# Optimization experiments

Hardware: AMD Instinct MI355X
Metric: run time of the kernel (lower is better)

## Reference

```python
import jax, jax.numpy as jnp
import numpy as np
import math
from jax.ops import segment_sum

TOPK_RATIO = 0.1
CLUSTER_RATIO = 0.25
K_KNN = 10


def setup_inputs() -> dict:
    key = jax.random.key(0)
    ks = jax.random.split(key, 10)
    N, C, H, W = 8, 256, 100, 352
    sc = 0.02
    return {
        "spatial_features_2d": jax.random.normal(ks[0], (N, C, H, W), jnp.float32),
        "dis_priority": jax.random.uniform(ks[1], (N, H, W), dtype=jnp.float32),
        "score_w1": jax.random.normal(ks[2], (256, 256), jnp.float32) * sc,
        "score_b1": jnp.zeros((256,), jnp.float32),
        "score_w2": jax.random.normal(ks[3], (1, 256), jnp.float32) * sc,
        "score_b2": jnp.zeros((1,), jnp.float32),
        "cls_w": jax.random.normal(ks[4], (2, 256), jnp.float32) * sc,
        "cls_b": jnp.zeros((2,), jnp.float32),
        "reg_w": jax.random.normal(ks[5], (14, 256), jnp.float32) * sc,
        "reg_b": jnp.zeros((14,), jnp.float32),
        "record_len": jnp.array([2, 3, 1, 2], jnp.int32),
    }


def _forward(x, dis_priority, score_w1, score_b1, score_w2, score_b2,
             cls_w, cls_b, reg_w, reg_b, record_len):
    N, C, H, W = x.shape
    L = H * W
    xf = x.reshape(N, C, L)  # [N,C,L]

    # --- SortSampler: per-pixel 2-layer fc score net (1x1 convs) ---
    h = jax.nn.relu(jnp.einsum('oc,ncl->nol', score_w1, xf) + score_b1[None, :, None])
    scores = jax.nn.sigmoid(jnp.einsum('oc,ncl->nol', score_w2, h) + score_b2[None, :, None])[:, 0]  # [N,L]
    weight = scores * dis_priority.reshape(N, L)
    K = max(int(math.ceil(L * TOPK_RATIO)), 1)  # static topk token count
    sort_idx = jnp.argsort(-weight, axis=1)[:, :K]              # pos_embed [N,K]
    conf = jnp.take_along_axis(weight, sort_idx, axis=1)        # [N,K]
    feats = jnp.take_along_axis(xf, sort_idx[:, None, :], axis=2)  # [N,C,K]
    src = jnp.transpose(feats, (0, 2, 1)) * conf[:, :, None]    # [N,K,C]

    # --- cluster_dpc_knn ---
    M = max(int(math.ceil(K * CLUSTER_RATIO)), 1)
    sq = jnp.sum(src * src, axis=-1)                             # [N,K]
    dist = sq[:, :, None] + sq[:, None, :] - 2.0 * jnp.einsum('nkc,njc->nkj', src, src)
    dist = jnp.maximum(dist, 0.0)                                # [N,K,K]
    dist_nearest = -jax.lax.top_k(-dist, K_KNN)[0]               # [N,K,k] smallest
    density = jnp.exp(-jnp.mean(dist_nearest, axis=-1))          # [N,K]
    density = density + jnp.arange(K, dtype=density.dtype) * 1e-6  # deterministic tie-break
    higher = density[:, None, :] > density[:, :, None]           # [N,K,K]
    dist_max = jnp.max(dist)
    d_higher = jnp.where(higher, dist, dist_max)
    delta = jnp.min(d_higher, axis=-1)                           # [N,K]
    score = delta * density
    idx_centers = jax.lax.top_k(score, M)[1]                     # [N,M]
    # assign each token to nearest cluster center
    dist_centers = jnp.take_along_axis(dist, idx_centers[:, :, None], axis=1)  # [N,M,K]
    idx_cluster = jnp.argmin(dist_centers, axis=1)               # [N,K]
    idx_cluster = idx_cluster.at[jnp.arange(N)[:, None], idx_centers].set(
        jnp.broadcast_to(jnp.arange(M), (N, M)))

    # --- merge_tokens: weighted average per cluster ---
    flat_seg = (idx_cluster + jnp.arange(N, dtype=idx_cluster.dtype)[:, None] * M).reshape(-1)
    w = conf.reshape(-1)
    all_w = segment_sum(w, flat_seg, num_segments=N * M) + 1e-6          # [N*M]
    merged = segment_sum((src * conf[:, :, None]).reshape(N * K, C), flat_seg,
                         num_segments=N * M) / all_w[:, None]
    merged = merged.reshape(N, M, C)
    # index_points: broadcast merged cluster feature back to each token
    src_tok = jnp.take_along_axis(merged, idx_cluster[:, :, None], axis=1)  # [N,K,C]
    src_ct = jnp.transpose(src_tok, (0, 2, 1))                   # [N,C,K]

    # --- scatter tokens back into BEV grid ---
    def scat(idxs, f):  # idxs [K], f [C,K]
        return jnp.zeros((C, L), f.dtype).at[:, idxs].set(f)
    bev = jax.vmap(scat)(sort_idx, src_ct)                       # [N,C,L]
    # ego CAVs (index 0 within each record) keep the full dense feature
    offsets = jnp.concatenate([jnp.zeros((1,), jnp.int32),
                               jnp.cumsum(record_len)[:-1].astype(jnp.int32)])
    is_ego = jnp.any(jnp.arange(N)[:, None] == offsets[None, :], axis=1)  # [N]
    bev = jnp.where(is_ego[:, None, None], xf, bev).reshape(N, C, H, W)

    # --- ego heads (1x1 convs) ---
    ego = x[offsets]                                              # [B,C,H,W]
    psm_ego = jnp.einsum('oc,bchw->bohw', cls_w, ego) + cls_b[None, :, None, None]
    rm_ego = jnp.einsum('oc,bchw->bohw', reg_w, ego) + reg_b[None, :, None, None]
    return bev, psm_ego, rm_ego


def reference(spatial_features_2d, dis_priority, score_w1, score_b1, score_w2, score_b2,
              cls_w, cls_b, reg_w, reg_b, record_len):
    return _forward(spatial_features_2d, dis_priority, score_w1, score_b1, score_w2,
                    score_b2, cls_w, cls_b, reg_w, reg_b, record_len)
```

## Files before the change

kernel.cpp:

```cpp
#include <hip/hip_runtime.h>
#include <hip/hip_bf16.h>

#define CCH   256
#define LPIX  35200
#define KSEL  3520
#define MCL   880
#define NBINS 16384
#define FMAXV 3.402823466e38f

typedef __bf16 bf16x8 __attribute__((ext_vector_type(8)));
typedef float  f32x4  __attribute__((ext_vector_type(4)));
typedef unsigned short ushort_t;

__device__ __forceinline__ void split3(float v, __bf16* h, __bf16* m, __bf16* l) {
    __bf16 a = (__bf16)v;
    float r = v - (float)a;
    __bf16 b = (__bf16)r;
    float r2 = r - (float)b;
    *h = a; *m = b; *l = (__bf16)r2;
}

#define MFMA6(ACC, AH, AM, AL, BH, BM, BL)                                   \
    ACC = __builtin_amdgcn_mfma_f32_16x16x32_bf16(AH, BH, ACC, 0, 0, 0);     \
    ACC = __builtin_amdgcn_mfma_f32_16x16x32_bf16(AH, BM, ACC, 0, 0, 0);     \
    ACC = __builtin_amdgcn_mfma_f32_16x16x32_bf16(AM, BH, ACC, 0, 0, 0);     \
    ACC = __builtin_amdgcn_mfma_f32_16x16x32_bf16(AH, BL, ACC, 0, 0, 0);     \
    ACC = __builtin_amdgcn_mfma_f32_16x16x32_bf16(AM, BM, ACC, 0, 0, 0);     \
    ACC = __builtin_amdgcn_mfma_f32_16x16x32_bf16(AL, BH, ACC, 0, 0, 0);

__global__ void split_w1(const float* __restrict__ w1, __bf16* __restrict__ h,
                         __bf16* __restrict__ m, __bf16* __restrict__ l) {
    int i = blockIdx.x * 256 + threadIdx.x;
    split3(w1[i], &h[i], &m[i], &l[i]);
}

__global__ __launch_bounds__(256) void score_mfma(
    const float* __restrict__ x, const float* __restrict__ prio,
    const __bf16* __restrict__ w1h, const __bf16* __restrict__ w1m, const __bf16* __restrict__ w1l,
    const float* __restrict__ b1, const float* __restrict__ w2, const float* __restrict__ b2,
    float* __restrict__ weight) {
    int n = blockIdx.y;
    int l0 = blockIdx.x * 64;
    int tid = threadIdx.x, w = tid >> 6, lane = tid & 63;
    int lrow = lane & 15, kg = lane >> 4;
    __shared__ __align__(16) __bf16 Xs[3][64][40];
    __shared__ float spart[64][17];
    const float* xb = x + (size_t)n * CCH * LPIX;
    f32x4 acc[4][4];
#pragma unroll
    for (int i = 0; i < 4; i++)
#pragma unroll
        for (int j = 0; j < 4; j++) acc[i][j] = (f32x4){0.f, 0.f, 0.f, 0.f};

    int cp = tid >> 4, lg = tid & 15;
    for (int c0 = 0; c0 < 256; c0 += 32) {
        __syncthreads();
        float4 f0 = *(const float4*)&xb[(size_t)(c0 + 2 * cp) * LPIX + l0 + lg * 4];
        float4 f1 = *(const float4*)&xb[(size_t)(c0 + 2 * cp + 1) * LPIX + l0 + lg * 4];
        float p0[4] = {f0.x, f0.y, f0.z, f0.w};
        float p1[4] = {f1.x, f1.y, f1.z, f1.w};
#pragma unroll
        for (int q = 0; q < 4; q++) {
            __bf16 h0, m0, lo0, h1, m1, lo1;
            split3(p0[q], &h0, &m0, &lo0);
            split3(p1[q], &h1, &m1, &lo1);
            int l = lg * 4 + q;
            *(unsigned*)&Xs[0][l][2 * cp] = ((unsigned)*(ushort_t*)&h1 << 16) | *(ushort_t*)&h0;
            *(unsigned*)&Xs[1][l][2 * cp] = ((unsigned)*(ushort_t*)&m1 << 16) | *(ushort_t*)&m0;
            *(unsigned*)&Xs[2][l][2 * cp] = ((unsigned)*(ushort_t*)&lo1 << 16) | *(ushort_t*)&lo0;
        }
        __syncthreads();
        bf16x8 bfh[4], bfm[4], bfl[4];
#pragma unroll
        for (int fj = 0; fj < 4; fj++) {
            bfh[fj] = *(const bf16x8*)&Xs[0][fj * 16 + lrow][kg * 8];
            bfm[fj] = *(const bf16x8*)&Xs[1][fj * 16 + lrow][kg * 8];
            bfl[fj] = *(const bf16x8*)&Xs[2][fj * 16 + lrow][kg * 8];
        }
#pragma unroll
        for (int fi = 0; fi < 4; fi++) {
            size_t ao = (size_t)(w * 64 + fi * 16 + lrow) * 256 + c0 + kg * 8;
            bf16x8 ah = *(const bf16x8*)&w1h[ao];
            bf16x8 am = *(const bf16x8*)&w1m[ao];
            bf16x8 al = *(const bf16x8*)&w1l[ao];
#pragma unroll
            for (int fj = 0; fj < 4; fj++) {
                MFMA6(acc[fi][fj], ah, am, al, bfh[fj], bfm[fj], bfl[fj]);
            }
        }
    }
    float ps[4] = {0.f, 0.f, 0.f, 0.f};
#pragma unroll
    for (int fi = 0; fi < 4; fi++) {
        int ob = w * 64 + fi * 16 + kg * 4;
        float4 b1v = *(const float4*)&b1[ob];
        float4 w2v = *(const float4*)&w2[ob];
        float b1a[4] = {b1v.x, b1v.y, b1v.z, b1v.w};
        float w2a[4] = {w2v.x, w2v.y, w2v.z, w2v.w};
#pragma unroll
        for (int r = 0; r < 4; r++)
#pragma unroll
            for (int fj = 0; fj < 4; fj++)
                ps[fj] += w2a[r] * fmaxf(acc[fi][fj][r] + b1a[r], 0.f);
    }
#pragma unroll
    for (int fj = 0; fj < 4; fj++) spart[fj * 16 + lrow][w * 4 + kg] = ps[fj];
    __syncthreads();
    if (tid < 64) {
        float s = 0.f;
#pragma unroll
        for (int r = 0; r < 16; r++) s += spart[tid][r];
        s += b2[0];
        float sg = 1.f / (1.f + expf(-s));
        weight[(size_t)n * LPIX + l0 + tid] = sg * prio[(size_t)n * LPIX + l0 + tid];
    }
}

__global__ void hist_kernel(const float* __restrict__ weight, int* __restrict__ hist) {
    int n = blockIdx.y;
    int i = blockIdx.x * 256 + threadIdx.x;
    if (i >= LPIX) return;
    float w = weight[(size_t)n * LPIX + i];
    int b = (int)(w * (float)NBINS);
    b = min(max(b, 0), NBINS - 1);
    atomicAdd(&hist[(size_t)n * NBINS + b], 1);
}

__global__ __launch_bounds__(256) void thr_kernel(const int* __restrict__ hist, int* __restrict__ thrbin) {
    int n = blockIdx.x, t = threadIdx.x;
    const int CH = NBINS / 256;
    __shared__ int csum[256];
    __shared__ int bfound;
    int base = NBINS - (t + 1) * CH;
    int s = 0;
    for (int i = 0; i < CH; i++) s += hist[(size_t)n * NBINS + base + i];
    csum[t] = s;
    __syncthreads();
    if (t == 0) {
        int cum = 0, sel = 255;
        for (int u = 0; u < 256; u++) {
            cum += csum[u];
            csum[u] = cum;
            if (cum >= KSEL) { sel = u; break; }
        }
        bfound = sel;
    }
    __syncthreads();
    if (t == 0) {
        int u = bfound;
        int cumBefore = (u == 0) ? 0 : csum[u - 1];
        int base2 = NBINS - (u + 1) * CH;
        int cum = cumBefore, bsel = base2;
        for (int b = base2 + CH - 1; b >= base2; b--) {
            cum += hist[(size_t)n * NBINS + b];
            if (cum >= KSEL) { bsel = b; break; }
        }
        thrbin[n] = bsel;
    }
}

__global__ void cand_kernel(const float* __restrict__ weight, const int* __restrict__ thrbin,
                            float* __restrict__ candw, int* __restrict__ cidx, int* __restrict__ ccnt) {
    int n = blockIdx.y;
    int i = blockIdx.x * 256 + threadIdx.x;
    if (i >= LPIX) return;
    float w = weight[(size_t)n * LPIX + i];
    int b = (int)(w * (float)NBINS);
    b = min(max(b, 0), NBINS - 1);
    if (b >= thrbin[n]) {
        int p = atomicAdd(&ccnt[n], 1);
        candw[(size_t)n * LPIX + p] = w;
        cidx[(size_t)n * LPIX + p] = i;
    }
}

__global__ __launch_bounds__(256) void rank_kernel(const float* __restrict__ candw, const int* __restrict__ cidx,
                                                   const int* __restrict__ ccnt,
                                                   float* __restrict__ conf, int* __restrict__ sidx) {
    int n = blockIdx.y, i = blockIdx.x;
    int cnt = ccnt[n];
    if (i >= cnt) return;
    float wi = candw[(size_t)n * LPIX + i];
    int ii = cidx[(size_t)n * LPIX + i];
    int r = 0;
    for (int j = threadIdx.x; j < cnt; j += 256) {
        float wj = candw[(size_t)n * LPIX + j];
        int ij = cidx[(size_t)n * LPIX + j];
        if (wj > wi || (wj == wi && ij < ii)) r++;
    }
    __shared__ int red[256];
    red[threadIdx.x] = r;
    __syncthreads();
    for (int s = 128; s > 0; s >>= 1) {
        if (threadIdx.x < s) red[threadIdx.x] += red[threadIdx.x + s];
        __syncthreads();
    }
    if (threadIdx.x == 0) {
        int rank = red[0];
        if (rank < KSEL) {
            sidx[(size_t)n * KSEL + rank] = ii;
            conf[(size_t)n * KSEL + rank] = wi;
        }
    }
}

__global__ __launch_bounds__(256) void gather_src(const float* __restrict__ x, const int* __restrict__ sidx,
                                                  const float* __restrict__ conf,
                                                  float* __restrict__ src,
                                                  __bf16* __restrict__ sh, __bf16* __restrict__ sm,
                                                  __bf16* __restrict__ sl,
                                                  float* __restrict__ sq, int* __restrict__ inv) {
    int n = blockIdx.y, k = blockIdx.x, c = threadIdx.x;
    int idx = sidx[(size_t)n * KSEL + k];
    float cf = conf[(size_t)n * KSEL + k];
    float v = x[((size_t)n * CCH + c) * LPIX + idx] * cf;
    size_t o = ((size_t)n * KSEL + k) * CCH + c;
    src[o] = v;
    __bf16 h, m, l;
    split3(v, &h, &m, &l);
    sh[o] = h; sm[o] = m; sl[o] = l;
    __shared__ float red[256];
    red[c] = v * v;
    __syncthreads();
    for (int s = 128; s > 0; s >>= 1) {
        if (c < s) red[c] += red[c + s];
        __syncthreads();
    }
    if (c == 0) {
        sq[(size_t)n * KSEL + k] = red[0];
        inv[(size_t)n * LPIX + idx] = k;
    }
}

__global__ __launch_bounds__(256) void dist_mfma(
    const __bf16* __restrict__ sh, const __bf16* __restrict__ sm, const __bf16* __restrict__ sl,
    const float* __restrict__ sq, float* __restrict__ dist, int n0) {
    int n = n0 + blockIdx.z;
    const size_t nbase = (size_t)n * KSEL * CCH;
    const float* sqn = sq + (size_t)n * KSEL;
    float* D = dist + (size_t)blockIdx.z * KSEL * KSEL;
    int b = blockIdx.x;
    int iT = (int)((sqrtf(8.f * (float)b + 1.f) - 1.f) * 0.5f);
    while ((iT + 1) * (iT + 2) / 2 <= b) iT++;
    while (iT * (iT + 1) / 2 > b) iT--;
    int jT = b - iT * (iT + 1) / 2;
    int bi = iT * 128, bj = jT * 128;
    __shared__ __align__(16) __bf16 As[3][128][40], Bs[3][128][40];
    int tid = threadIdx.x, w = tid >> 6, lane = tid & 63;
    int lrow = lane & 15, kg = lane >> 4;
    int wr = w >> 1, wc = w & 1;
    f32x4 acc[4][4];
#pragma unroll
    for (int i = 0; i < 4; i++)
#pragma unroll
        for (int j = 0; j < 4; j++) acc[i][j] = (f32x4){0.f, 0.f, 0.f, 0.f};

    int sr = tid & 127, g2 = tid >> 7;
    size_t ra = nbase + (size_t)min(bi + sr, KSEL - 1) * CCH;
    size_t rb = nbase + (size_t)min(bj + sr, KSEL - 1) * CCH;

    bf16x8 rA[3][2], rB[3][2];
#pragma unroll
    for (int s2 = 0; s2 < 2; s2++) {
        int cg = s2 * 2 + g2;
        rA[0][s2] = *(const bf16x8*)&sh[ra + cg * 8];
        rA[1][s2] = *(const bf16x8*)&sm[ra + cg * 8];
        rA[2][s2] = *(const bf16x8*)&sl[ra + cg * 8];
        rB[0][s2] = *(const bf16x8*)&sh[rb + cg * 8];
        rB[1][s2] = *(const bf16x8*)&sm[rb + cg * 8];
        rB[2][s2] = *(const bf16x8*)&sl[rb + cg * 8];
    }
    for (int c0 = 0; c0 < 256; c0 += 32) {
        __syncthreads();
#pragma unroll
        for (int s2 = 0; s2 < 2; s2++) {
            int cg = s2 * 2 + g2;
            *(bf16x8*)&As[0][sr][cg * 8] = rA[0][s2];
            *(bf16x8*)&As[1][sr][cg * 8] = rA[1][s2];
            *(bf16x8*)&As[2][sr][cg * 8] = rA[2][s2];
            *(bf16x8*)&Bs[0][sr][cg * 8] = rB[0][s2];
            *(bf16x8*)&Bs[1][sr][cg * 8] = rB[1][s2];
            *(bf16x8*)&Bs[2][sr][cg * 8] = rB[2][s2];
        }
        __syncthreads();
        if (c0 < 224) {
            int c1 = c0 + 32;
#pragma unroll
            for (int s2 = 0; s2 < 2; s2++) {
                int cg = s2 * 2 + g2;
                rA[0][s2] = *(const bf16x8*)&sh[ra + c1 + cg * 8];
                rA[1][s2] = *(const bf16x8*)&sm[ra + c1 + cg * 8];
                rA[2][s2] = *(const bf16x8*)&sl[ra + c1 + cg * 8];
                rB[0][s2] = *(const bf16x8*)&sh[rb + c1 + cg * 8];
                rB[1][s2] = *(const bf16x8*)&sm[rb + c1 + cg * 8];
                rB[2][s2] = *(const bf16x8*)&sl[rb + c1 + cg * 8];
            }
        }
        bf16x8 bfh[4], bfm[4], bfl[4];
#pragma unroll
        for (int fj = 0; fj < 4; fj++) {
            bfh[fj] = *(const bf16x8*)&Bs[0][wc * 64 + fj * 16 + lrow][kg * 8];
            bfm[fj] = *(const bf16x8*)&Bs[1][wc * 64 + fj * 16 + lrow][kg * 8];
            bfl[fj] = *(const bf16x8*)&Bs[2][wc * 64 + fj * 16 + lrow][kg * 8];
        }
#pragma unroll
        for (int fi = 0; fi < 4; fi++) {
            int arow = wr * 64 + fi * 16 + lrow;
            bf16x8 ah = *(const bf16x8*)&As[0][arow][kg * 8];
            bf16x8 am = *(const bf16x8*)&As[1][arow][kg * 8];
            bf16x8 al = *(const bf16x8*)&As[2][arow][kg * 8];
#pragma unroll
            for (int fj = 0; fj < 4; fj++) {
                MFMA6(acc[fi][fj], ah, am, al, bfh[fj], bfm[fj], bfl[fj]);
            }
        }
    }
#pragma unroll
    for (int fi = 0; fi < 4; fi++) {
        int gi0 = bi + wr * 64 + fi * 16;
        if (gi0 >= KSEL) continue;
        float4 siv = *(const float4*)&sqn[gi0 + kg * 4];
        float sia[4] = {siv.x, siv.y, siv.z, siv.w};
#pragma unroll
        for (int fj = 0; fj < 4; fj++) {
            int gj0 = bj + wc * 64 + fj * 16;
            if (gj0 >= KSEL) continue;
            int gj = gj0 + lrow;
            float sj = sqn[gj];
            float dv[4];
#pragma unroll
            for (int r = 0; r < 4; r++) {
                int gi = gi0 + kg * 4 + r;
                dv[r] = fmaxf(sia[r] + sj - 2.f * acc[fi][fj][r], 0.f);
                D[(size_t)gi * KSEL + gj] = dv[r];
            }
            if (iT != jT) {
                *(float4*)&D[(size_t)gj * KSEL + gi0 + kg * 4] = *(float4*)dv;
            }
        }
    }
}

__global__ __launch_bounds__(256) void knn_density(const float* __restrict__ dist, float* __restrict__ density, int n0) {
    int n = n0 + blockIdx.y;
    int row = threadIdx.x >> 6;
    int lane = threadIdx.x & 63;
    int i = blockIdx.x * 4 + row;
    const float4* row4 = (const float4*)(dist + (size_t)blockIdx.y * KSEL * KSEL + (size_t)i * KSEL);
    float tt[10];
#pragma unroll
    for (int r = 0; r < 10; r++) tt[r] = FMAXV;
    for (int j4 = lane; j4 < KSEL / 4; j4 += 64) {
        float4 v4 = row4[j4];
        float vv[4] = {v4.x, v4.y, v4.z, v4.w};
#pragma unroll
        for (int q = 0; q < 4; q++) {
            float v = vv[q];
            if (v < tt[9]) {
                tt[9] = v;
#pragma unroll
                for (int r = 9; r > 0; r--) {
                    if (tt[r] < tt[r - 1]) { float tmp = tt[r - 1]; tt[r - 1] = tt[r]; tt[r] = tmp; }
                }
            }
        }
    }
    __shared__ float ls[4][64][10];
#pragma unroll
    for (int r = 0; r < 10; r++) ls[row][lane][r] = tt[r];
    __syncthreads();
    for (int s = 32; s >= 1; s >>= 1) {
        if (lane < s) {
            float out[10];
            int ia = 0, ib = 0;
#pragma unroll
            for (int r = 0; r < 10; r++) {
                float va = ls[row][lane][ia], vb = ls[row][lane + s][ib];
                if (va <= vb) { out[r] = va; ia++; } else { out[r] = vb; ib++; }
            }
#pragma unroll
            for (int r = 0; r < 10; r++) ls[row][lane][r] = out[r];
        }
        __syncthreads();
    }
    if (lane == 0) {
        float sum = 0.f;
#pragma unroll
        for (int r = 0; r < 10; r++) sum += ls[row][0][r];
        density[(size_t)n * KSEL + i] = expf(-sum * 0.1f) + (float)i * 1e-6f;
    }
}

__global__ __launch_bounds__(256) void delta_score(const float* __restrict__ dist, const float* __restrict__ density,
                                                   float* __restrict__ scoreb, int n0) {
    int n = n0 + blockIdx.y;
    int i = blockIdx.x;
    const float4* row = (const float4*)(dist + (size_t)blockIdx.y * KSEL * KSEL + (size_t)i * KSEL);
    const float* dn = density + (size_t)n * KSEL;
    const float4* dn4 = (const float4*)dn;
    float di = dn[i];
    float mn = FMAXV;
    for (int j4 = threadIdx.x; j4 < KSEL / 4; j4 += 256) {
        float4 d = dn4[j4];
        float4 v = row[j4];
        if (d.x > di) mn = fminf(mn, v.x);
        if (d.y > di) mn = fminf(mn, v.y);
        if (d.z > di) mn = fminf(mn, v.z);
        if (d.w > di) mn = fminf(mn, v.w);
    }
    __shared__ float red[256];
    red[threadIdx.x] = mn;
    __syncthreads();
    for (int s = 128; s > 0; s >>= 1) {
        if (threadIdx.x < s) red[threadIdx.x] = fminf(red[threadIdx.x], red[threadIdx.x + s]);
        __syncthreads();
    }
    if (threadIdx.x == 0) {
        float d = red[0];
        scoreb[(size_t)n * KSEL + i] = (d == FMAXV) ? FMAXV : d * di;
    }
}

__global__ __launch_bounds__(256) void center_rank(const float* __restrict__ scoreb, int* __restrict__ centers,
                                                   int* __restrict__ crank, int n0) {
    int n = n0 + blockIdx.y;
    int i = blockIdx.x;
    const float* sc = scoreb + (size_t)n * KSEL;
    float si = sc[i];
    int r = 0;
    for (int j = threadIdx.x; j < KSEL; j += 256) {
        float sj = sc[j];
        if (sj > si || (sj == si && j < i)) r++;
    }
    __shared__ int red[256];
    red[threadIdx.x] = r;
    __syncthreads();
    for (int s = 128; s > 0; s >>= 1) {
        if (threadIdx.x < s) red[threadIdx.x] += red[threadIdx.x + s];
        __syncthreads();
    }
    if (threadIdx.x == 0) {
        int rank = red[0];
        if (rank < MCL) {
            centers[(size_t)n * MCL + rank] = i;
            crank[(size_t)n * KSEL + i] = rank;
        }
    }
}

__global__ __launch_bounds__(256) void assign_kernel(const float* __restrict__ dist, const int* __restrict__ centers,
                                                     const int* __restrict__ crank, const float* __restrict__ conf,
                                                     int* __restrict__ clus, float* __restrict__ allw, int n0) {
    int n = n0 + blockIdx.y;
    const float* D = dist + (size_t)blockIdx.y * KSEL * KSEL;
    int kl = threadIdx.x & 63, mc = threadIdx.x >> 6;
    int k = blockIdx.x * 64 + kl;
    const int* ctr = centers + (size_t)n * MCL;
    float mn = FMAXV;
    int am = MCL;
    for (int m = mc * 220; m < (mc + 1) * 220; m++) {
        float v = D[(size_t)ctr[m] * KSEL + k];
        if (v < mn) { mn = v; am = m; }
    }
    __shared__ float mv[4][64];
    __shared__ int mi[4][64];
    mv[mc][kl] = mn;
    mi[mc][kl] = am;
    __syncthreads();
    if (mc == 0) {
        float best = mv[0][kl];
        int bm = mi[0][kl];
#pragma unroll
        for (int c = 1; c < 4; c++) {
            float v = mv[c][kl];
            int im = mi[c][kl];
            if (v < best || (v == best && im < bm)) { best = v; bm = im; }
        }
        int cr = crank[(size_t)n * KSEL + k];
        int cl = (cr >= 0) ? cr : bm;
        clus[(size_t)n * KSEL + k] = cl;
        atomicAdd(&allw[(size_t)n * MCL + cl], conf[(size_t)n * KSEL + k]);
    }
}

__global__ void merge_feat(const float* __restrict__ src, const float* __restrict__ conf,
                           const int* __restrict__ clus, float* __restrict__ merged, int n0) {
    int n = n0 + blockIdx.y;
    int k = blockIdx.x, c = threadIdx.x;
    float v = src[((size_t)n * KSEL + k) * CCH + c] * conf[(size_t)n * KSEL + k];
    atomicAdd(&merged[((size_t)n * MCL + clus[(size_t)n * KSEL + k]) * CCH + c], v);
}

__global__ void merged_div(float* __restrict__ merged, const float* __restrict__ allw) {
    int nm = blockIdx.x, c = threadIdx.x;
    merged[(size_t)nm * CCH + c] /= (allw[nm] + 1e-6f);
}

__global__ __launch_bounds__(256) void bev_kernel(const float* __restrict__ x, const int* __restrict__ inv,
                                                  const int* __restrict__ clus, const float* __restrict__ merged,
                                                  const int* __restrict__ reclen, int B, float* __restrict__ out) {
    int n = blockIdx.y;
    int l0 = (blockIdx.x * 256 + threadIdx.x) * 4;
    if (l0 >= LPIX) return;
    bool ego = false;
    {
        int off = 0;
        for (int b = 0; b < B; b++) {
            if (n == off) { ego = true; break; }
            off += reclen[b];
        }
    }
    size_t base = (size_t)n * CCH * LPIX + l0;
    if (ego) {
        for (int c = 0; c < CCH; c++)
            *(float4*)&out[base + (size_t)c * LPIX] = *(const float4*)&x[base + (size_t)c * LPIX];
    } else {
        const float* mr0; const float* mr1; const float* mr2; const float* mr3;
        {
            int t0 = inv[(size_t)n * LPIX + l0 + 0];
            int t1 = inv[(size_t)n * LPIX + l0 + 1];
            int t2 = inv[(size_t)n * LPIX + l0 + 2];
            int t3 = inv[(size_t)n * LPIX + l0 + 3];
            mr0 = (t0 >= 0) ? merged + ((size_t)n * MCL + clus[(size_t)n * KSEL + t0]) * CCH : nullptr;
            mr1 = (t1 >= 0) ? merged + ((size_t)n * MCL + clus[(size_t)n * KSEL + t1]) * CCH : nullptr;
            mr2 = (t2 >= 0) ? merged + ((size_t)n * MCL + clus[(size_t)n * KSEL + t2]) * CCH : nullptr;
            mr3 = (t3 >= 0) ? merged + ((size_t)n * MCL + clus[(size_t)n * KSEL + t3]) * CCH : nullptr;
        }
        for (int c = 0; c < CCH; c++) {
            float4 v;
            v.x = mr0 ? mr0[c] : 0.f;
            v.y = mr1 ? mr1[c] : 0.f;
            v.z = mr2 ? mr2[c] : 0.f;
            v.w = mr3 ? mr3[c] : 0.f;
            *(float4*)&out[base + (size_t)c * LPIX] = v;
        }
    }
}

__global__ __launch_bounds__(256) void heads_kernel(const float* __restrict__ x,
                                                    const float* __restrict__ clsw, const float* __restrict__ clsb,
                                                    const float* __restrict__ regw, const float* __restrict__ regb,
                                                    const int* __restrict__ reclen,
                                                    float* __restrict__ psm, float* __restrict__ rm) {
    int b = blockIdx.y;
    int l0 = (blockIdx.x * 256 + threadIdx.x) * 4;
    __shared__ float ws[16][256];
    __shared__ float bs[16];
    for (int i = threadIdx.x; i < 16 * 256; i += 256) {
        int o = i >> 8, c = i & 255;
        ws[o][c] = (o < 2) ? clsw[o * 256 + c] : regw[(o - 2) * 256 + c];
    }
    if (threadIdx.x < 16) bs[threadIdx.x] = (threadIdx.x < 2) ? clsb[threadIdx.x] : regb[threadIdx.x - 2];
    __syncthreads();
    if (l0 >= LPIX) return;
    int off = 0;
    for (int u = 0; u < b; u++) off += reclen[u];
    const float* xb = x + (size_t)off * CCH * LPIX;
    float acc[16][4] = {};
    for (int c = 0; c < CCH; c++) {
        float4 v = *(const float4*)&xb[(size_t)c * LPIX + l0];
#pragma unroll
        for (int o = 0; o < 16; o++) {
            float w = ws[o][c];
            acc[o][0] += w * v.x; acc[o][1] += w * v.y; acc[o][2] += w * v.z; acc[o][3] += w * v.w;
        }
    }
#pragma unroll
    for (int o = 0; o < 2; o++) {
        float4 r;
        r.x = acc[o][0] + bs[o]; r.y = acc[o][1] + bs[o]; r.z = acc[o][2] + bs[o]; r.w = acc[o][3] + bs[o];
        *(float4*)&psm[((size_t)b * 2 + o) * LPIX + l0] = r;
    }
#pragma unroll
    for (int o = 0; o < 14; o++) {
        float4 r;
        float bb = bs[o + 2];
        r.x = acc[o + 2][0] + bb; r.y = acc[o + 2][1] + bb; r.z = acc[o + 2][2] + bb; r.w = acc[o + 2][3] + bb;
        *(float4*)&rm[((size_t)b * 14 + o) * LPIX + l0] = r;
    }
}

extern "C" void kernel_launch(void* const* d_in, const int* in_sizes, int n_in,
                              void* d_out, int out_size, void* d_ws, size_t ws_size,
                              hipStream_t stream) {
    const float* x    = (const float*)d_in[0];
    const float* prio = (const float*)d_in[1];
    const float* w1   = (const float*)d_in[2];
    const float* b1   = (const float*)d_in[3];
    const float* w2   = (const float*)d_in[4];
    const float* b2   = (const float*)d_in[5];
    const float* clsw = (const float*)d_in[6];
    const float* clsb = (const float*)d_in[7];
    const float* regw = (const float*)d_in[8];
    const float* regb = (const float*)d_in[9];
    const int* reclen = (const int*)d_in[10];
    int N = in_sizes[0] / (CCH * LPIX);
    int B = in_sizes[10];
    float* out = (float*)d_out;

    char* p = (char*)d_ws;
    size_t off = 0;
    auto alloc = [&](size_t bytes) -> void* {
        void* r = p + off;
        off += (bytes + 255) & ~(size_t)255;
        return r;
    };
    __bf16* w1h    = (__bf16*)alloc(256 * 256 * 2);
    __bf16* w1m    = (__bf16*)alloc(256 * 256 * 2);
    __bf16* w1l    = (__bf16*)alloc(256 * 256 * 2);
    float* weight  = (float*)alloc((size_t)N * LPIX * 4);
    int*   hist    = (int*)alloc((size_t)N * NBINS * 4);
    int*   thrbin  = (int*)alloc((size_t)N * 4);
    int*   ccnt    = (int*)alloc((size_t)N * 4);
    float* candw   = (float*)alloc((size_t)N * LPIX * 4);
    int*   cidx    = (int*)alloc((size_t)N * LPIX * 4);
    int*   sidx    = (int*)alloc((size_t)N * KSEL * 4);
    float* conf    = (float*)alloc((size_t)N * KSEL * 4);
    float* src     = (float*)alloc((size_t)N * KSEL * CCH * 4);
    __bf16* srch   = (__bf16*)alloc((size_t)N * KSEL * CCH * 2);
    __bf16* srcm   = (__bf16*)alloc((size_t)N * KSEL * CCH * 2);
    __bf16* srcl   = (__bf16*)alloc((size_t)N * KSEL * CCH * 2);
    float* sq      = (float*)alloc((size_t)N * KSEL * 4);
    int*   inv     = (int*)alloc((size_t)N * LPIX * 4);
    float* density = (float*)alloc((size_t)N * KSEL * 4);
    float* scoreb  = (float*)alloc((size_t)N * KSEL * 4);
    int*   centers = (int*)alloc((size_t)N * MCL * 4);
    int*   crank   = (int*)alloc((size_t)N * KSEL * 4);
    int*   clus    = (int*)alloc((size_t)N * KSEL * 4);
    float* allw    = (float*)alloc((size_t)N * MCL * 4);
    float* merged  = (float*)alloc((size_t)N * MCL * CCH * 4);
    const size_t distB = (size_t)KSEL * KSEL * 4;
    size_t rem = (ws_size > off) ? (ws_size - off) : 0;
    int nd = (int)(rem / distB);
    if (nd < 1) nd = 1;
    if (nd > N) nd = N;
    float* dist = (float*)alloc(distB * nd);

    hipMemsetAsync(hist, 0, (size_t)N * NBINS * 4, stream);
    hipMemsetAsync(ccnt, 0, (size_t)N * 4, stream);
    hipMemsetAsync(inv, 0xFF, (size_t)N * LPIX * 4, stream);
    hipMemsetAsync(crank, 0xFF, (size_t)N * KSEL * 4, stream);
    hipMemsetAsync(allw, 0, (size_t)N * MCL * 4, stream);
    hipMemsetAsync(merged, 0, (size_t)N * MCL * CCH * 4, stream);

    split_w1<<<256, 256, 0, stream>>>(w1, w1h, w1m, w1l);
    score_mfma<<<dim3(LPIX / 64, N), 256, 0, stream>>>(x, prio, w1h, w1m, w1l, b1, w2, b2, weight);
    hist_kernel<<<dim3((LPIX + 255) / 256, N), 256, 0, stream>>>(weight, hist);
    thr_kernel<<<N, 256, 0, stream>>>(hist, thrbin);
    cand_kernel<<<dim3((LPIX + 255) / 256, N), 256, 0, stream>>>(weight, thrbin, candw, cidx, ccnt);
    rank_kernel<<<dim3(8192, N), 256, 0, stream>>>(candw, cidx, ccnt, conf, sidx);
    gather_src<<<dim3(KSEL, N), 256, 0, stream>>>(x, sidx, conf, src, srch, srcm, srcl, sq, inv);

    const int TI = (KSEL + 127) / 128;
    const int NT = TI * (TI + 1) / 2;
    for (int g = 0; g < N; g += nd) {
        int nb = (N - g < nd) ? (N - g) : nd;
        dist_mfma<<<dim3(NT, 1, nb), 256, 0, stream>>>(srch, srcm, srcl, sq, dist, g);
        knn_density<<<dim3(KSEL / 4, nb), 256, 0, stream>>>(dist, density, g);
        delta_score<<<dim3(KSEL, nb), 256, 0, stream>>>(dist, density, scoreb, g);
        center_rank<<<dim3(KSEL, nb), 256, 0, stream>>>(scoreb, centers, crank, g);
        assign_kernel<<<dim3(KSEL / 64, nb), 256, 0, stream>>>(dist, centers, crank, conf, clus, allw, g);
        merge_feat<<<dim3(KSEL, nb), 256, 0, stream>>>(src, conf, clus, merged, g);
    }
    merged_div<<<N * MCL, 256, 0, stream>>>(merged, allw);
    bev_kernel<<<dim3((LPIX / 4 + 255) / 256, N), 256, 0, stream>>>(x, inv, clus, merged, reclen, B, out);

    float* psm = out + (size_t)N * CCH * LPIX;
    float* rm  = psm + (size_t)B * 2 * LPIX;
    heads_kernel<<<dim3((LPIX / 4 + 255) / 256, B), 256, 0, stream>>>(x, clsw, clsb, regw, regb, reclen, psm, rm);
}
```

Measured before the change: 1.403 ms.

## Double-buffer score GEMM staging and fuse ego heads into BEV copy

The score MFMA kernel now double-buffers its shared-memory X tiles and prefetches the next chunk's global X and W1 fragments while the current chunk's MFMAs run, with one barrier per iteration instead of two. The ego-head 1x1 convolutions are folded into the BEV kernel's ego copy path, so the ego features are read from global memory once instead of twice and one launch is removed. The distance batch size is also capped at 4 samples per group. The prefetching adds register pressure (12 W1 fragments per buffer), which could lower occupancy, and every BEV block now carries 16KB of shared memory.

```diff
diff --git a/kernel.cpp b/kernel.cpp
--- a/kernel.cpp
+++ b/kernel.cpp
@@ -43,7 +43,7 @@
     int l0 = blockIdx.x * 64;
     int tid = threadIdx.x, w = tid >> 6, lane = tid & 63;
     int lrow = lane & 15, kg = lane >> 4;
-    __shared__ __align__(16) __bf16 Xs[3][64][40];
+    __shared__ __align__(16) __bf16 Xs[2][3][64][40];
     __shared__ float spart[64][17];
     const float* xb = x + (size_t)n * CCH * LPIX;
     f32x4 acc[4][4];
@@ -53,42 +53,68 @@
         for (int j = 0; j < 4; j++) acc[i][j] = (f32x4){0.f, 0.f, 0.f, 0.f};
 
     int cp = tid >> 4, lg = tid & 15;
-    for (int c0 = 0; c0 < 256; c0 += 32) {
-        __syncthreads();
-        float4 f0 = *(const float4*)&xb[(size_t)(c0 + 2 * cp) * LPIX + l0 + lg * 4];
-        float4 f1 = *(const float4*)&xb[(size_t)(c0 + 2 * cp + 1) * LPIX + l0 + lg * 4];
-        float p0[4] = {f0.x, f0.y, f0.z, f0.w};
-        float p1[4] = {f1.x, f1.y, f1.z, f1.w};
+
+    auto loadx = [&](int k, float4* dst) {
+        int c0 = k * 32;
+        dst[0] = *(const float4*)&xb[(size_t)(c0 + 2 * cp) * LPIX + l0 + lg * 4];
+        dst[1] = *(const float4*)&xb[(size_t)(c0 + 2 * cp + 1) * LPIX + l0 + lg * 4];
+    };
+    auto loadw = [&](int k, bf16x8* dst) {
+#pragma unroll
+        for (int fi = 0; fi < 4; fi++) {
+            size_t ao = (size_t)(w * 64 + fi * 16 + lrow) * 256 + k * 32 + kg * 8;
+            dst[fi * 3 + 0] = *(const bf16x8*)&w1h[ao];
+            dst[fi * 3 + 1] = *(const bf16x8*)&w1m[ao];
+            dst[fi * 3 + 2] = *(const bf16x8*)&w1l[ao];
+        }
+    };
+    auto stage = [&](int buf, const float4* pfv) {
+        float p0[4] = {pfv[0].x, pfv[0].y, pfv[0].z, pfv[0].w};
+        float p1[4] = {pfv[1].x, pfv[1].y, pfv[1].z, pfv[1].w};
 #pragma unroll
         for (int q = 0; q < 4; q++) {
             __bf16 h0, m0, lo0, h1, m1, lo1;
             split3(p0[q], &h0, &m0, &lo0);
             split3(p1[q], &h1, &m1, &lo1);
             int l = lg * 4 + q;
-            *(unsigned*)&Xs[0][l][2 * cp] = ((unsigned)*(ushort_t*)&h1 << 16) | *(ushort_t*)&h0;
-            *(unsigned*)&Xs[1][l][2 * cp] = ((unsigned)*(ushort_t*)&m1 << 16) | *(ushort_t*)&m0;
-            *(unsigned*)&Xs[2][l][2 * cp] = ((unsigned)*(ushort_t*)&lo1 << 16) | *(ushort_t*)&lo0;
-        }
-        __syncthreads();
+            *(unsigned*)&Xs[buf][0][l][2 * cp] = ((unsigned)*(ushort_t*)&h1 << 16) | *(ushort_t*)&h0;
+            *(unsigned*)&Xs[buf][1][l][2 * cp] = ((unsigned)*(ushort_t*)&m1 << 16) | *(ushort_t*)&m0;
+            *(unsigned*)&Xs[buf][2][l][2 * cp] = ((unsigned)*(ushort_t*)&lo1 << 16) | *(ushort_t*)&lo0;
+        }
+    };
+
+    float4 pf[2][2];
+    bf16x8 wfr[2][12];
+    loadx(0, pf[0]);
+    loadw(0, wfr[0]);
+    stage(0, pf[0]);
+    loadx(1, pf[1]);
+    __syncthreads();
+
+#pragma unroll
+    for (int k = 0; k < 8; k++) {
+        const int buf = k & 1;
         bf16x8 bfh[4], bfm[4], bfl[4];
 #pragma unroll
         for (int fj = 0; fj < 4; fj++) {
-            bfh[fj] = *(const bf16x8*)&Xs[0][fj * 16 + lrow][kg * 8];
-            bfm[fj] = *(const bf16x8*)&Xs[1][fj * 16 + lrow][kg * 8];
-            bfl[fj] = *(const bf16x8*)&Xs[2][fj * 16 + lrow][kg * 8];
-        }
+            bfh[fj] = *(const bf16x8*)&Xs[buf][0][fj * 16 + lrow][kg * 8];
+            bfm[fj] = *(const bf16x8*)&Xs[buf][1][fj * 16 + lrow][kg * 8];
+            bfl[fj] = *(const bf16x8*)&Xs[buf][2][fj * 16 + lrow][kg * 8];
+        }
+        if (k < 7) loadw(k + 1, wfr[buf ^ 1]);
+        if (k < 6) loadx(k + 2, pf[buf]);
+        if (k < 7) stage(buf ^ 1, pf[buf ^ 1]);
 #pragma unroll
         for (int fi = 0; fi < 4; fi++) {
-            size_t ao = (size_t)(w * 64 + fi * 16 + lrow) * 256 + c0 + kg * 8;
-            bf16x8 ah = *(const bf16x8*)&w1h[ao];
-            bf16x8 am = *(const bf16x8*)&w1m[ao];
-            bf16x8 al = *(const bf16x8*)&w1l[ao];
 #pragma unroll
             for (int fj = 0; fj < 4; fj++) {
-                MFMA6(acc[fi][fj], ah, am, al, bfh[fj], bfm[fj], bfl[fj]);
-            }
-        }
-    }
+                MFMA6(acc[fi][fj], wfr[buf][fi * 3 + 0], wfr[buf][fi * 3 + 1],
+                      wfr[buf][fi * 3 + 2], bfh[fj], bfm[fj], bfl[fj]);
+            }
+        }
+        __syncthreads();
+    }
+
     float ps[4] = {0.f, 0.f, 0.f, 0.f};
 #pragma unroll
     for (int fi = 0; fi < 4; fi++) {
@@ -498,22 +524,58 @@
 
 __global__ __launch_bounds__(256) void bev_kernel(const float* __restrict__ x, const int* __restrict__ inv,
                                                   const int* __restrict__ clus, const float* __restrict__ merged,
-                                                  const int* __restrict__ reclen, int B, float* __restrict__ out) {
+                                                  const int* __restrict__ reclen, int B,
+                                                  const float* __restrict__ clsw, const float* __restrict__ clsb,
+                                                  const float* __restrict__ regw, const float* __restrict__ regb,
+                                                  float* __restrict__ out, float* __restrict__ psm,
+                                                  float* __restrict__ rm) {
     int n = blockIdx.y;
     int l0 = (blockIdx.x * 256 + threadIdx.x) * 4;
-    if (l0 >= LPIX) return;
     bool ego = false;
+    int bego = 0;
     {
         int off = 0;
         for (int b = 0; b < B; b++) {
-            if (n == off) { ego = true; break; }
+            if (n == off) { ego = true; bego = b; break; }
             off += reclen[b];
         }
     }
+    __shared__ float ws[16][256];
+    __shared__ float bs[16];
+    if (ego) {
+        for (int i = threadIdx.x; i < 16 * 256; i += 256) {
+            int o = i >> 8, c = i & 255;
+            ws[o][c] = (o < 2) ? clsw[o * 256 + c] : regw[(o - 2) * 256 + c];
+        }
+        if (threadIdx.x < 16) bs[threadIdx.x] = (threadIdx.x < 2) ? clsb[threadIdx.x] : regb[threadIdx.x - 2];
+        __syncthreads();
+    }
+    if (l0 >= LPIX) return;
     size_t base = (size_t)n * CCH * LPIX + l0;
     if (ego) {
-        for (int c = 0; c < CCH; c++)
-            *(float4*)&out[base + (size_t)c * LPIX] = *(const float4*)&x[base + (size_t)c * LPIX];
+        float acc[16][4] = {};
+        for (int c = 0; c < CCH; c++) {
+            float4 v = *(const float4*)&x[base + (size_t)c * LPIX];
+            *(float4*)&out[base + (size_t)c * LPIX] = v;
+#pragma unroll
+            for (int o = 0; o < 16; o++) {
+                float wv = ws[o][c];
+                acc[o][0] += wv * v.x; acc[o][1] += wv * v.y; acc[o][2] += wv * v.z; acc[o][3] += wv * v.w;
+            }
+        }
+#pragma unroll
+        for (int o = 0; o < 2; o++) {
+            float4 r;
+            r.x = acc[o][0] + bs[o]; r.y = acc[o][1] + bs[o]; r.z = acc[o][2] + bs[o]; r.w = acc[o][3] + bs[o];
+            *(float4*)&psm[((size_t)bego * 2 + o) * LPIX + l0] = r;
+        }
+#pragma unroll
+        for (int o = 0; o < 14; o++) {
+            float4 r;
+            float bb = bs[o + 2];
+            r.x = acc[o + 2][0] + bb; r.y = acc[o + 2][1] + bb; r.z = acc[o + 2][2] + bb; r.w = acc[o + 2][3] + bb;
+            *(float4*)&rm[((size_t)bego * 14 + o) * LPIX + l0] = r;
+        }
     } else {
         const float* mr0; const float* mr1; const float* mr2; const float* mr3;
         {
@@ -534,49 +596,6 @@
             v.w = mr3 ? mr3[c] : 0.f;
             *(float4*)&out[base + (size_t)c * LPIX] = v;
         }
-    }
-}
-
-__global__ __launch_bounds__(256) void heads_kernel(const float* __restrict__ x,
-                                                    const float* __restrict__ clsw, const float* __restrict__ clsb,
-                                                    const float* __restrict__ regw, const float* __restrict__ regb,
-                                                    const int* __restrict__ reclen,
-                                                    float* __restrict__ psm, float* __restrict__ rm) {
-    int b = blockIdx.y;
-    int l0 = (blockIdx.x * 256 + threadIdx.x) * 4;
-    __shared__ float ws[16][256];
-    __shared__ float bs[16];
-    for (int i = threadIdx.x; i < 16 * 256; i += 256) {
-        int o = i >> 8, c = i & 255;
-        ws[o][c] = (o < 2) ? clsw[o * 256 + c] : regw[(o - 2) * 256 + c];
-    }
-    if (threadIdx.x < 16) bs[threadIdx.x] = (threadIdx.x < 2) ? clsb[threadIdx.x] : regb[threadIdx.x - 2];
-    __syncthreads();
-    if (l0 >= LPIX) return;
-    int off = 0;
-    for (int u = 0; u < b; u++) off += reclen[u];
-    const float* xb = x + (size_t)off * CCH * LPIX;
-    float acc[16][4] = {};
-    for (int c = 0; c < CCH; c++) {
-        float4 v = *(const float4*)&xb[(size_t)c * LPIX + l0];
-#pragma unroll
-        for (int o = 0; o < 16; o++) {
-            float w = ws[o][c];
-            acc[o][0] += w * v.x; acc[o][1] += w * v.y; acc[o][2] += w * v.z; acc[o][3] += w * v.w;
-        }
-    }
-#pragma unroll
-    for (int o = 0; o < 2; o++) {
-        float4 r;
-        r.x = acc[o][0] + bs[o]; r.y = acc[o][1] + bs[o]; r.z = acc[o][2] + bs[o]; r.w = acc[o][3] + bs[o];
-        *(float4*)&psm[((size_t)b * 2 + o) * LPIX + l0] = r;
-    }
-#pragma unroll
-    for (int o = 0; o < 14; o++) {
-        float4 r;
-        float bb = bs[o + 2];
-        r.x = acc[o + 2][0] + bb; r.y = acc[o + 2][1] + bb; r.z = acc[o + 2][2] + bb; r.w = acc[o + 2][3] + bb;
-        *(float4*)&rm[((size_t)b * 14 + o) * LPIX + l0] = r;
     }
 }
 
@@ -634,6 +653,7 @@
     int nd = (int)(rem / distB);
     if (nd < 1) nd = 1;
     if (nd > N) nd = N;
+    if (nd > 4) nd = 4;
     float* dist = (float*)alloc(distB * nd);
 
     hipMemsetAsync(hist, 0, (size_t)N * NBINS * 4, stream);
@@ -663,9 +683,9 @@
         merge_feat<<<dim3(KSEL, nb), 256, 0, stream>>>(src, conf, clus, merged, g);
     }
     merged_div<<<N * MCL, 256, 0, stream>>>(merged, allw);
-    bev_kernel<<<dim3((LPIX / 4 + 255) / 256, N), 256, 0, stream>>>(x, inv, clus, merged, reclen, B, out);
 
     float* psm = out + (size_t)N * CCH * LPIX;
     float* rm  = psm + (size_t)B * 2 * LPIX;
-    heads_kernel<<<dim3((LPIX / 4 + 255) / 256, B), 256, 0, stream>>>(x, clsw, clsb, regw, regb, reclen, psm, rm);
-}
+    bev_kernel<<<dim3((LPIX / 4 + 255) / 256, N), 256, 0, stream>>>(
+        x, inv, clus, merged, reclen, B, clsw, clsb, regw, regb, out, psm, rm);
+}
```

Result: faster. 1.310 ms (-6.7%).
